# Kernel tuning notes

Hardware: AMD Instinct MI355X
Metric: run time of the kernel (lower is better)

The kernel has to match this reference:

```python
import jax, jax.numpy as jnp
import numpy as np

DIM = 1024
NUM_HEADS = 16


def setup_inputs() -> dict:
    key = jax.random.key(0)
    ks = jax.random.split(key, 8)
    B, N, C = 2, 2048, DIM
    x = jax.random.normal(ks[0], (B, N, C), dtype=jnp.float32)
    attn_mask = jnp.zeros((B, 1, N, N), dtype=jnp.float32)
    # learned parameters
    w_qkv = jax.random.normal(ks[1], (3 * C, C), dtype=jnp.float32) * (C ** -0.5)
    q_bias = jnp.zeros((C,), dtype=jnp.float32)
    k_bias = jnp.zeros((C,), dtype=jnp.float32)
    v_bias = jnp.zeros((C,), dtype=jnp.float32)
    w_proj = jax.random.normal(ks[2], (C, C), dtype=jnp.float32) * (C ** -0.5)
    b_proj = jnp.zeros((C,), dtype=jnp.float32)
    return {
        "x": x, "attn_mask": attn_mask,
        "w_qkv": w_qkv, "q_bias": q_bias, "k_bias": k_bias, "v_bias": v_bias,
        "w_proj": w_proj, "b_proj": b_proj,
        "num_heads": NUM_HEADS,
    }


def reference(x, attn_mask, w_qkv, q_bias, k_bias, v_bias, w_proj, b_proj, num_heads):
    B, N, C = x.shape
    H = num_heads
    hd = C // H
    scale = hd ** -0.5
    alpha = 32.0
    # fused qkv projection with concatenated biases
    qkv_bias = jnp.concatenate([q_bias, k_bias, v_bias])
    qkv = x @ w_qkv.T + qkv_bias                       # [B, N, 3C]
    qkv = qkv.reshape(B, N, 3, H, hd).transpose(2, 0, 3, 1, 4)  # [3, B, H, N, hd]
    q, k, v = qkv[0], qkv[1], qkv[2]
    # stabilization trick: scale q down by alpha, compute scores, re-scale after max-subtraction
    q = q * (scale / alpha)
    attn = jnp.einsum('bhld,bhmd->bhlm', q, k)         # [B, H, N, N]
    attn = (attn - jnp.max(attn, axis=-1, keepdims=True)) * alpha
    attn = attn + attn_mask                            # additive mask, broadcast over heads
    attn = jax.nn.softmax(attn, axis=-1)
    out = jnp.einsum('bhlm,bhmd->blhd', attn, v).reshape(B, N, C)
    out = out @ w_proj.T + b_proj
    return out
```

## Files before the change

kernel.cpp:

```cpp
#include <hip/hip_runtime.h>

typedef unsigned short u16;
typedef __bf16   bf16x8 __attribute__((ext_vector_type(8)));
typedef float    f32x4  __attribute__((ext_vector_type(4)));
typedef float    f32x16 __attribute__((ext_vector_type(16)));
typedef unsigned u32x4v __attribute__((ext_vector_type(4)));
typedef u16      u16x8  __attribute__((ext_vector_type(8)));

#define DEV __device__ __forceinline__

DEV u16 tobf(float f) {
  return __builtin_bit_cast(unsigned short, (__bf16)f);
}

DEV unsigned pack2(float a, float b) {
  return (unsigned)tobf(a) | ((unsigned)tobf(b) << 16);
}

DEV f32x4 fzero() { f32x4 z; z[0]=0.f; z[1]=0.f; z[2]=0.f; z[3]=0.f; return z; }

DEV void async_cp16(void* lds, const void* g) {
  __builtin_amdgcn_global_load_lds(
      (const __attribute__((address_space(1))) void*)g,
      (__attribute__((address_space(3))) void*)lds, 16, 0, 0);
}

DEV void cvt8(const float* __restrict__ in, u16* __restrict__ out, int i) {
  const float4* in4 = (const float4*)in;
  float4 a = in4[2*i], b = in4[2*i+1];
  u16x8 r;
  r[0]=tobf(a.x); r[1]=tobf(a.y); r[2]=tobf(a.z); r[3]=tobf(a.w);
  r[4]=tobf(b.x); r[5]=tobf(b.y); r[6]=tobf(b.z); r[7]=tobf(b.w);
  *(u16x8*)(out + 8*(size_t)i) = r;
}

__global__ __launch_bounds__(256)
void k_pre(const float* __restrict__ x, const float* __restrict__ wqkv,
           const float* __restrict__ wproj,
           u16* __restrict__ xb, u16* __restrict__ wqkvb, u16* __restrict__ wprojb,
           const u32x4v* __restrict__ mask, unsigned* __restrict__ flag)
{
  const int tid = blockIdx.x * blockDim.x + threadIdx.x;
  const int stride = gridDim.x * blockDim.x;
  for (int i = tid; i < 524288; i += stride) cvt8(x, xb, i);
  for (int i = tid; i < 393216; i += stride) cvt8(wqkv, wqkvb, i);
  for (int i = tid; i < 131072; i += stride) cvt8(wproj, wprojb, i);
  unsigned o = 0;
  for (int i = tid; i < 2097152; i += stride) {
    u32x4v v = mask[i];
    o |= v[0] | v[1] | v[2] | v[3];
  }
  if (o & 0x7fffffffu) atomicOr(flag, 1u);
}

template<int EPI>
__global__ __launch_bounds__(256)
void k_gemm_nt(const u16* __restrict__ A, const u16* __restrict__ B,
               int N, int K, int nbn,
               const float* __restrict__ bq, const float* __restrict__ bk,
               const float* __restrict__ bv,
               u16* __restrict__ qo, u16* __restrict__ ko, u16* __restrict__ vto,
               float* __restrict__ fo, const float* __restrict__ bp)
{
  __shared__ u16 sA[2][4096];
  __shared__ u16 sB[2][4096];

  const int tid  = threadIdx.x;
  const int lane = tid & 63;
  const int wave = tid >> 6;
  const int lr = lane & 15, lg = lane >> 4;
  const int wr = wave >> 1, wc = wave & 1;

  const int per = gridDim.x >> 3;
  const int bid = blockIdx.x;
  const int swz = (bid & 7) * per + (bid >> 3);
  const int bm0 = (swz / nbn) << 7;
  const int bn0 = (swz - (swz / nbn) * nbn) << 7;

  const size_t Kb = (size_t)K * 2;

  auto stage = [&](int buf, int kt) {
#pragma unroll
    for (int j = 0; j < 2; ++j) {
      int off = (tid + j * 256) << 4;
      int row = off >> 6;
      int ch  = (off & 63) >> 4;
      int gch = ch ^ (row & 3);
      async_cp16((char*)&sA[buf][0] + off,
                 (const char*)A + (size_t)(bm0 + row) * Kb + (size_t)kt * 64 + gch * 16);
      async_cp16((char*)&sB[buf][0] + off,
                 (const char*)B + (size_t)(bn0 + row) * Kb + (size_t)kt * 64 + gch * 16);
    }
  };

  f32x4 acc[4][4];
#pragma unroll
  for (int i = 0; i < 4; ++i)
#pragma unroll
    for (int j = 0; j < 4; ++j) acc[i][j] = fzero();

  const int nk = K >> 5;
  stage(0, 0);

  for (int kt = 0; kt < nk; ++kt) {
    const int cur = kt & 1;
    if (kt + 1 < nk) {
      stage(cur ^ 1, kt + 1);
      asm volatile("s_waitcnt vmcnt(4)" ::: "memory");
    } else {
      asm volatile("s_waitcnt vmcnt(0)" ::: "memory");
    }
    __builtin_amdgcn_s_barrier();
    __builtin_amdgcn_sched_barrier(0);

    bf16x8 af[4], bfr[4];
#pragma unroll
    for (int mi = 0; mi < 4; ++mi) {
      int row = (wr << 6) + (mi << 4) + lr;
      int addr = (row << 6) + ((lg ^ (row & 3)) << 4);
      af[mi] = *(const bf16x8*)((const char*)&sA[cur][0] + addr);
    }
#pragma unroll
    for (int ni = 0; ni < 4; ++ni) {
      int row = (wc << 6) + (ni << 4) + lr;
      int addr = (row << 6) + ((lg ^ (row & 3)) << 4);
      bfr[ni] = *(const bf16x8*)((const char*)&sB[cur][0] + addr);
    }
    __builtin_amdgcn_s_setprio(1);
#pragma unroll
    for (int mi = 0; mi < 4; ++mi)
#pragma unroll
      for (int ni = 0; ni < 4; ++ni)
        acc[mi][ni] = __builtin_amdgcn_mfma_f32_16x16x32_bf16(af[mi], bfr[ni], acc[mi][ni], 0, 0, 0);
    __builtin_amdgcn_s_setprio(0);

    __builtin_amdgcn_s_barrier();
  }

#pragma unroll
  for (int mi = 0; mi < 4; ++mi) {
#pragma unroll
    for (int ni = 0; ni < 4; ++ni) {
      int col = bn0 + (wc << 6) + (ni << 4) + lr;
      if (EPI == 0) {
        int s = col >> 10, hd = col & 1023;
        int h = hd >> 6, d = hd & 63;
        float bias = (s == 0 ? bq[hd] : (s == 1 ? bk[hd] : bv[hd]));
#pragma unroll
        for (int r = 0; r < 4; ++r) {
          int m = bm0 + (wr << 6) + (mi << 4) + (lg << 2) + r;
          int b = m >> 11, n = m & 2047;
          float v = acc[mi][ni][r] + bias;
          if (s == 0) v *= 0.125f;
          u16 val = tobf(v);
          size_t bh = (size_t)(b * 16 + h);
          if (s == 0)      qo[(bh * 2048 + n) * 64 + d] = val;
          else if (s == 1) ko[(bh * 2048 + n) * 64 + d] = val;
          else             vto[(bh * 64 + d) * 2048 + n] = val;
        }
      } else {
        float bias = bp[col];
#pragma unroll
        for (int r = 0; r < 4; ++r) {
          int m = bm0 + (wr << 6) + (mi << 4) + (lg << 2) + r;
          fo[(size_t)m * N + col] = acc[mi][ni][r] + bias;
        }
      }
    }
  }
}

__global__ __launch_bounds__(256)
void k_attn(const u16* __restrict__ qb, const u16* __restrict__ kb,
            const u16* __restrict__ vtb, u16* __restrict__ ao,
            const float* __restrict__ mask, const unsigned* __restrict__ flag)
{
  constexpr int N = 2048;
  constexpr int NTT = N / 64;
  __shared__ u16 sK[4][4096];
  __shared__ u16 sV[4][4096];

  const int tid  = threadIdx.x;
  const int lane = tid & 63;
  const int wave = tid >> 6;
  const int l31  = lane & 31;
  const int hi   = lane >> 5;

  const int bid  = blockIdx.x;
  const int xcd  = bid & 7, slot = bid >> 3;
  const int bh   = xcd + 8 * (slot >> 4);
  const int qt   = slot & 15;
  const int b    = bh >> 4, h = bh & 15;

  const u16* Kbh = kb  + (size_t)bh * N * 64;
  const u16* Vbh = vtb + (size_t)bh * 64 * N;
  const int q_lo = qt * 128 + wave * 32;
  const int qg   = q_lo + l31;

  bf16x8 qf[4];
  {
    const u16* qrow = qb + ((size_t)bh * N + qg) * 64;
#pragma unroll
    for (int ks = 0; ks < 4; ++ks)
      qf[ks] = *(const bf16x8*)(qrow + ks * 16 + hi * 8);
  }

  const unsigned use_mask = *flag;
  const float* maskb = mask + (size_t)b * N * N;

  float m_run = -INFINITY, lsum = 0.f;
  f32x16 o0, o1;
#pragma unroll
  for (int r = 0; r < 16; ++r) { o0[r] = 0.f; o1[r] = 0.f; }

  auto stage = [&](int buf, int kt) {
#pragma unroll
    for (int j = 0; j < 2; ++j) {
      int off = (tid + j * 256) << 4;
      int row = off >> 7;
      int ch  = (off & 127) >> 4;
      int gch = ch ^ (row & 7);
      async_cp16((char*)&sK[buf][0] + off,
                 (const char*)Kbh + (size_t)(kt * 64 + row) * 128 + gch * 16);
      async_cp16((char*)&sV[buf][0] + off,
                 (const char*)Vbh + (size_t)row * (N * 2) + (size_t)kt * 128 + gch * 16);
    }
  };

  stage(0, 0);
  stage(1, 1);

  const float L2E = 1.44269504088896340736f;

  for (int kt = 0; kt < NTT; ++kt) {
    const int cur = kt & 3;
    if (kt + 2 < NTT) stage((kt + 2) & 3, kt + 2);
    if (kt + 2 < NTT)      asm volatile("s_waitcnt vmcnt(8)" ::: "memory");
    else if (kt + 1 < NTT) asm volatile("s_waitcnt vmcnt(4)" ::: "memory");
    else                   asm volatile("s_waitcnt vmcnt(0)" ::: "memory");
    __builtin_amdgcn_s_barrier();
    __builtin_amdgcn_sched_barrier(0);

    const char* kbase = (const char*)&sK[cur][0];
    const char* vbase = (const char*)&sV[cur][0];

    f32x16 sc0, sc1;
#pragma unroll
    for (int r = 0; r < 16; ++r) { sc0[r] = 0.f; sc1[r] = 0.f; }

    __builtin_amdgcn_s_setprio(1);
#pragma unroll
    for (int ks = 0; ks < 4; ++ks) {
      int row0 = l31;
      int a0 = (row0 << 7) + ((((ks << 1) + hi) ^ (row0 & 7)) << 4);
      bf16x8 kf0 = *(const bf16x8*)(kbase + a0);
      sc0 = __builtin_amdgcn_mfma_f32_32x32x16_bf16(kf0, qf[ks], sc0, 0, 0, 0);
      int row1 = 32 + l31;
      int a1 = (row1 << 7) + ((((ks << 1) + hi) ^ (row1 & 7)) << 4);
      bf16x8 kf1 = *(const bf16x8*)(kbase + a1);
      sc1 = __builtin_amdgcn_mfma_f32_32x32x16_bf16(kf1, qf[ks], sc1, 0, 0, 0);
    }
    __builtin_amdgcn_s_setprio(0);

    if (use_mask) {
#pragma unroll
      for (int r = 0; r < 16; ++r) {
        int krow = (r & 3) + 8 * (r >> 2) + 4 * hi;
        sc0[r] += maskb[(size_t)qg * N + kt * 64 + krow];
        sc1[r] += maskb[(size_t)qg * N + kt * 64 + 32 + krow];
      }
    }

    float tmx[8];
#pragma unroll
    for (int r = 0; r < 8; ++r)
      tmx[r] = fmaxf(fmaxf(sc0[r], sc0[r + 8]), fmaxf(sc1[r], sc1[r + 8]));
#pragma unroll
    for (int r = 0; r < 4; ++r) tmx[r] = fmaxf(tmx[r], tmx[r + 4]);
    float pm = fmaxf(fmaxf(tmx[0], tmx[1]), fmaxf(tmx[2], tmx[3]));
    pm = fmaxf(pm, __shfl_xor(pm, 32, 64));

    if (__any(pm > m_run + 8.f)) {
      const float m_new = fmaxf(m_run, pm);
      const float f = __builtin_amdgcn_exp2f((m_run - m_new) * L2E);
      m_run = m_new;
#pragma unroll
      for (int r = 0; r < 16; ++r) {
        float fr = __shfl(f, (r & 3) + 8 * (r >> 2) + 4 * hi, 64);
        o0[r] *= fr; o1[r] *= fr;
      }
      lsum *= f;
    }

    const float mL2 = m_run * L2E;
    float rs0 = 0.f, rs1 = 0.f, rs2 = 0.f, rs3 = 0.f;
#pragma unroll
    for (int r = 0; r < 16; r += 4) {
      sc0[r]   = __builtin_amdgcn_exp2f(__builtin_fmaf(sc0[r],   L2E, -mL2));
      sc0[r+1] = __builtin_amdgcn_exp2f(__builtin_fmaf(sc0[r+1], L2E, -mL2));
      sc0[r+2] = __builtin_amdgcn_exp2f(__builtin_fmaf(sc0[r+2], L2E, -mL2));
      sc0[r+3] = __builtin_amdgcn_exp2f(__builtin_fmaf(sc0[r+3], L2E, -mL2));
      sc1[r]   = __builtin_amdgcn_exp2f(__builtin_fmaf(sc1[r],   L2E, -mL2));
      sc1[r+1] = __builtin_amdgcn_exp2f(__builtin_fmaf(sc1[r+1], L2E, -mL2));
      sc1[r+2] = __builtin_amdgcn_exp2f(__builtin_fmaf(sc1[r+2], L2E, -mL2));
      sc1[r+3] = __builtin_amdgcn_exp2f(__builtin_fmaf(sc1[r+3], L2E, -mL2));
      rs0 += sc0[r]   + sc1[r];
      rs1 += sc0[r+1] + sc1[r+1];
      rs2 += sc0[r+2] + sc1[r+2];
      rs3 += sc0[r+3] + sc1[r+3];
    }
    float rs = (rs0 + rs1) + (rs2 + rs3);
    rs += __shfl_xor(rs, 32, 64);
    lsum += rs;

    unsigned P32_0[8], P32_1[8];
#pragma unroll
    for (int tt = 0; tt < 8; ++tt) {
      P32_0[tt] = pack2(sc0[2 * tt], sc0[2 * tt + 1]);
      P32_1[tt] = pack2(sc1[2 * tt], sc1[2 * tt + 1]);
    }

    bf16x8 pa[4];
#pragma unroll
    for (int ks16 = 0; ks16 < 4; ++ks16) {
      const int b4 = (ks16 & 1) << 2;
      unsigned c0, c1, c2, c3;
      if (ks16 < 2) { c0 = P32_0[b4]; c2 = P32_0[b4+2]; c1 = P32_0[b4+1]; c3 = P32_0[b4+3]; }
      else          { c0 = P32_1[b4]; c2 = P32_1[b4+2]; c1 = P32_1[b4+1]; c3 = P32_1[b4+3]; }
      asm volatile("v_permlane32_swap_b32 %0, %1" : "+v"(c0), "+v"(c2));
      asm volatile("v_permlane32_swap_b32 %0, %1" : "+v"(c1), "+v"(c3));
      u32x4v w; w[0] = c0; w[1] = c1; w[2] = c2; w[3] = c3;
      pa[ks16] = __builtin_bit_cast(bf16x8, w);
    }

    __builtin_amdgcn_s_setprio(1);
#pragma unroll
    for (int ks16 = 0; ks16 < 4; ++ks16) {
      int row0 = l31;
      int a0 = (row0 << 7) + ((((ks16 << 1) + hi) ^ (row0 & 7)) << 4);
      bf16x8 vf0 = *(const bf16x8*)(vbase + a0);
      o0 = __builtin_amdgcn_mfma_f32_32x32x16_bf16(pa[ks16], vf0, o0, 0, 0, 0);
      int row1 = 32 + l31;
      int a1 = (row1 << 7) + ((((ks16 << 1) + hi) ^ (row1 & 7)) << 4);
      bf16x8 vf1 = *(const bf16x8*)(vbase + a1);
      o1 = __builtin_amdgcn_mfma_f32_32x32x16_bf16(pa[ks16], vf1, o1, 0, 0, 0);
    }
    __builtin_amdgcn_s_setprio(0);
  }

  const float inv = 1.0f / lsum;
#pragma unroll
  for (int r = 0; r < 16; ++r) {
    int idx = (r & 3) + 8 * (r >> 2) + 4 * hi;
    float ivr = __shfl(inv, idx, 64);
    int qrow = q_lo + idx;
    size_t base = ((size_t)(b * N + qrow)) * 1024 + h * 64;
    ao[base + l31]      = tobf(o0[r] * ivr);
    ao[base + 32 + l31] = tobf(o1[r] * ivr);
  }
}

extern "C" void kernel_launch(void* const* d_in, const int* in_sizes, int n_in,
                              void* d_out, int out_size, void* d_ws, size_t ws_size,
                              hipStream_t stream) {
  const float* x      = (const float*)d_in[0];
  const float* mask   = (const float*)d_in[1];
  const float* w_qkv  = (const float*)d_in[2];
  const float* q_bias = (const float*)d_in[3];
  const float* k_bias = (const float*)d_in[4];
  const float* v_bias = (const float*)d_in[5];
  const float* w_proj = (const float*)d_in[6];
  const float* b_proj = (const float*)d_in[7];
  float* out = (float*)d_out;

  const int B = 2, N = 2048, C = 1024;
  const int M = B * N;

  u16* ws     = (u16*)d_ws;
  u16* xb     = ws;
  u16* wqkvb  = ws + 4194304;
  u16* wprojb = ws + 7340032;
  u16* qbuf   = ws + 8388608;
  u16* kbuf   = ws + 12582912;
  u16* vtbuf  = ws + 16777216;
  unsigned* flag = (unsigned*)(ws + 20971520);
  u16* aob    = xb;

  hipMemsetAsync(flag, 0, 4, stream);
  k_pre<<<2048, 256, 0, stream>>>(x, w_qkv, w_proj, xb, wqkvb, wprojb,
                                  (const u32x4v*)mask, flag);

  k_gemm_nt<0><<<(M / 128) * (3 * C / 128), 256, 0, stream>>>(
      xb, wqkvb, 3 * C, C, 3 * C / 128,
      q_bias, k_bias, v_bias, qbuf, kbuf, vtbuf, nullptr, nullptr);

  k_attn<<<B * 16 * (N / 128), 256, 0, stream>>>(qbuf, kbuf, vtbuf, aob, mask, flag);

  k_gemm_nt<1><<<(M / 128) * (C / 128), 256, 0, stream>>>(
      aob, wprojb, C, C, C / 128,
      nullptr, nullptr, nullptr, nullptr, nullptr, nullptr, out, b_proj);
}
```

Before: 144.0 us.

## Software-pipeline attention loop: compute next tile's QK^T during current softmax/PV

Restructures the flash-attention inner loop so the QK^T MFMAs for tile t+1 are issued before the softmax and PV work for tile t, with score accumulators ping-ponged between two register sets. Wait counts are tightened so tile t+1 is resident in LDS before its scores are computed. The aim is to overlap matrix-core work with the exp/max/pack VALU work. It costs extra accumulator registers, which may reduce occupancy or cause spills.

```diff
diff --git a/kernel.cpp b/kernel.cpp
--- a/kernel.cpp
+++ b/kernel.cpp
@@ -227,41 +227,28 @@
     }
   };
 
-  stage(0, 0);
-  stage(1, 1);
-
-  const float L2E = 1.44269504088896340736f;
-
-  for (int kt = 0; kt < NTT; ++kt) {
-    const int cur = kt & 3;
-    if (kt + 2 < NTT) stage((kt + 2) & 3, kt + 2);
-    if (kt + 2 < NTT)      asm volatile("s_waitcnt vmcnt(8)" ::: "memory");
-    else if (kt + 1 < NTT) asm volatile("s_waitcnt vmcnt(4)" ::: "memory");
-    else                   asm volatile("s_waitcnt vmcnt(0)" ::: "memory");
-    __builtin_amdgcn_s_barrier();
-    __builtin_amdgcn_sched_barrier(0);
-
-    const char* kbase = (const char*)&sK[cur][0];
-    const char* vbase = (const char*)&sV[cur][0];
-
-    f32x16 sc0, sc1;
-#pragma unroll
-    for (int r = 0; r < 16; ++r) { sc0[r] = 0.f; sc1[r] = 0.f; }
-
+  auto qk = [&](int kt, f32x16& d0, f32x16& d1) {
+    const char* kbase = (const char*)&sK[kt & 3][0];
+#pragma unroll
+    for (int r = 0; r < 16; ++r) { d0[r] = 0.f; d1[r] = 0.f; }
     __builtin_amdgcn_s_setprio(1);
 #pragma unroll
     for (int ks = 0; ks < 4; ++ks) {
       int row0 = l31;
       int a0 = (row0 << 7) + ((((ks << 1) + hi) ^ (row0 & 7)) << 4);
       bf16x8 kf0 = *(const bf16x8*)(kbase + a0);
-      sc0 = __builtin_amdgcn_mfma_f32_32x32x16_bf16(kf0, qf[ks], sc0, 0, 0, 0);
+      d0 = __builtin_amdgcn_mfma_f32_32x32x16_bf16(kf0, qf[ks], d0, 0, 0, 0);
       int row1 = 32 + l31;
       int a1 = (row1 << 7) + ((((ks << 1) + hi) ^ (row1 & 7)) << 4);
       bf16x8 kf1 = *(const bf16x8*)(kbase + a1);
-      sc1 = __builtin_amdgcn_mfma_f32_32x32x16_bf16(kf1, qf[ks], sc1, 0, 0, 0);
+      d1 = __builtin_amdgcn_mfma_f32_32x32x16_bf16(kf1, qf[ks], d1, 0, 0, 0);
     }
     __builtin_amdgcn_s_setprio(0);
-
+  };
+
+  const float L2E = 1.44269504088896340736f;
+
+  auto smpv = [&](int kt, f32x16& sc0, f32x16& sc1) {
     if (use_mask) {
 #pragma unroll
       for (int r = 0; r < 16; ++r) {
@@ -333,6 +320,7 @@
       pa[ks16] = __builtin_bit_cast(bf16x8, w);
     }
 
+    const char* vbase = (const char*)&sV[kt & 3][0];
     __builtin_amdgcn_s_setprio(1);
 #pragma unroll
     for (int ks16 = 0; ks16 < 4; ++ks16) {
@@ -346,6 +334,31 @@
       o1 = __builtin_amdgcn_mfma_f32_32x32x16_bf16(pa[ks16], vf1, o1, 0, 0, 0);
     }
     __builtin_amdgcn_s_setprio(0);
+  };
+
+  stage(0, 0);
+  stage(1, 1);
+  asm volatile("s_waitcnt vmcnt(4)" ::: "memory");
+  __builtin_amdgcn_s_barrier();
+  __builtin_amdgcn_sched_barrier(0);
+
+  f32x16 scA0, scA1, scB0, scB1;
+  qk(0, scA0, scA1);
+
+#pragma unroll 2
+  for (int t = 0; t < NTT; ++t) {
+    if (t + 2 < NTT) stage((t + 2) & 3, t + 2);
+    if (t + 2 < NTT)      asm volatile("s_waitcnt vmcnt(4)" ::: "memory");
+    else                  asm volatile("s_waitcnt vmcnt(0)" ::: "memory");
+    __builtin_amdgcn_s_barrier();
+    __builtin_amdgcn_sched_barrier(0);
+
+    if (t + 1 < NTT) qk(t + 1, scB0, scB1);
+    smpv(t, scA0, scA1);
+
+    f32x16 u0 = scA0, u1 = scA1;
+    scA0 = scB0; scA1 = scB1;
+    scB0 = u0;  scB1 = u1;
   }
 
   const float inv = 1.0f / lsum;
```

Measured after the change: 145.2 us. No clear change (+0.9%).

## Split attention KV range across two blocks and merge partials in a new kernel

Applied to the files above, without the earlier changes.

Splits each query tile's key range into two halves handled by separate blocks, doubling the grid from 512 to 1024 blocks so more CUs are occupied. Each block writes an unnormalized-then-normalized partial output plus its row max and sum, and a new merge kernel combines the two halves with softmax rescaling. The K/V pipeline is reduced from a 4-buffer depth-2 prefetch with fine-grained waitcnt to double buffering with __syncthreads, and launch bounds request higher occupancy. This adds an extra kernel launch, extra global traffic for the partials, and bf16 rounding of intermediate partials.

```diff
diff --git a/kernel.cpp b/kernel.cpp
--- a/kernel.cpp
+++ b/kernel.cpp
@@ -11,6 +11,10 @@
 
 DEV u16 tobf(float f) {
   return __builtin_bit_cast(unsigned short, (__bf16)f);
+}
+
+DEV float frombf(u16 u) {
+  return (float)__builtin_bit_cast(__bf16, u);
 }
 
 DEV unsigned pack2(float a, float b) {
@@ -170,15 +174,15 @@
   }
 }
 
-__global__ __launch_bounds__(256)
+__global__ __launch_bounds__(256, 4)
 void k_attn(const u16* __restrict__ qb, const u16* __restrict__ kb,
-            const u16* __restrict__ vtb, u16* __restrict__ ao,
+            const u16* __restrict__ vtb, u16* __restrict__ pa,
+            float2* __restrict__ stats,
             const float* __restrict__ mask, const unsigned* __restrict__ flag)
 {
   constexpr int N = 2048;
-  constexpr int NTT = N / 64;
-  __shared__ u16 sK[4][4096];
-  __shared__ u16 sV[4][4096];
+  __shared__ u16 sK[2][4096];
+  __shared__ u16 sV[2][4096];
 
   const int tid  = threadIdx.x;
   const int lane = tid & 63;
@@ -188,9 +192,12 @@
 
   const int bid  = blockIdx.x;
   const int xcd  = bid & 7, slot = bid >> 3;
-  const int bh   = xcd + 8 * (slot >> 4);
-  const int qt   = slot & 15;
-  const int b    = bh >> 4, h = bh & 15;
+  const int g    = slot & 1;
+  const int s2   = slot >> 1;
+  const int bh   = xcd + 8 * (s2 >> 4);
+  const int qt   = s2 & 15;
+  const int b    = bh >> 4;
+  const int kt0  = g << 4;
 
   const u16* Kbh = kb  + (size_t)bh * N * 64;
   const u16* Vbh = vtb + (size_t)bh * 64 * N;
@@ -227,19 +234,15 @@
     }
   };
 
-  stage(0, 0);
-  stage(1, 1);
+  stage(0, kt0);
+  __syncthreads();
 
   const float L2E = 1.44269504088896340736f;
 
-  for (int kt = 0; kt < NTT; ++kt) {
-    const int cur = kt & 3;
-    if (kt + 2 < NTT) stage((kt + 2) & 3, kt + 2);
-    if (kt + 2 < NTT)      asm volatile("s_waitcnt vmcnt(8)" ::: "memory");
-    else if (kt + 1 < NTT) asm volatile("s_waitcnt vmcnt(4)" ::: "memory");
-    else                   asm volatile("s_waitcnt vmcnt(0)" ::: "memory");
-    __builtin_amdgcn_s_barrier();
-    __builtin_amdgcn_sched_barrier(0);
+  for (int tt = 0; tt < 16; ++tt) {
+    const int kt  = kt0 + tt;
+    const int cur = tt & 1;
+    if (tt + 1 < 16) stage(cur ^ 1, kt + 1);
 
     const char* kbase = (const char*)&sK[cur][0];
     const char* vbase = (const char*)&sV[cur][0];
@@ -315,12 +318,12 @@
 
     unsigned P32_0[8], P32_1[8];
 #pragma unroll
-    for (int tt = 0; tt < 8; ++tt) {
-      P32_0[tt] = pack2(sc0[2 * tt], sc0[2 * tt + 1]);
-      P32_1[tt] = pack2(sc1[2 * tt], sc1[2 * tt + 1]);
-    }
-
-    bf16x8 pa[4];
+    for (int pt = 0; pt < 8; ++pt) {
+      P32_0[pt] = pack2(sc0[2 * pt], sc0[2 * pt + 1]);
+      P32_1[pt] = pack2(sc1[2 * pt], sc1[2 * pt + 1]);
+    }
+
+    bf16x8 paf[4];
 #pragma unroll
     for (int ks16 = 0; ks16 < 4; ++ks16) {
       const int b4 = (ks16 & 1) << 2;
@@ -330,7 +333,7 @@
       asm volatile("v_permlane32_swap_b32 %0, %1" : "+v"(c0), "+v"(c2));
       asm volatile("v_permlane32_swap_b32 %0, %1" : "+v"(c1), "+v"(c3));
       u32x4v w; w[0] = c0; w[1] = c1; w[2] = c2; w[3] = c3;
-      pa[ks16] = __builtin_bit_cast(bf16x8, w);
+      paf[ks16] = __builtin_bit_cast(bf16x8, w);
     }
 
     __builtin_amdgcn_s_setprio(1);
@@ -339,25 +342,58 @@
       int row0 = l31;
       int a0 = (row0 << 7) + ((((ks16 << 1) + hi) ^ (row0 & 7)) << 4);
       bf16x8 vf0 = *(const bf16x8*)(vbase + a0);
-      o0 = __builtin_amdgcn_mfma_f32_32x32x16_bf16(pa[ks16], vf0, o0, 0, 0, 0);
+      o0 = __builtin_amdgcn_mfma_f32_32x32x16_bf16(paf[ks16], vf0, o0, 0, 0, 0);
       int row1 = 32 + l31;
       int a1 = (row1 << 7) + ((((ks16 << 1) + hi) ^ (row1 & 7)) << 4);
       bf16x8 vf1 = *(const bf16x8*)(vbase + a1);
-      o1 = __builtin_amdgcn_mfma_f32_32x32x16_bf16(pa[ks16], vf1, o1, 0, 0, 0);
+      o1 = __builtin_amdgcn_mfma_f32_32x32x16_bf16(paf[ks16], vf1, o1, 0, 0, 0);
     }
     __builtin_amdgcn_s_setprio(0);
+
+    __syncthreads();
   }
 
   const float inv = 1.0f / lsum;
+  u16* pab = pa + (size_t)g * 4194304;
 #pragma unroll
   for (int r = 0; r < 16; ++r) {
     int idx = (r & 3) + 8 * (r >> 2) + 4 * hi;
     float ivr = __shfl(inv, idx, 64);
     int qrow = q_lo + idx;
-    size_t base = ((size_t)(b * N + qrow)) * 1024 + h * 64;
-    ao[base + l31]      = tobf(o0[r] * ivr);
-    ao[base + 32 + l31] = tobf(o1[r] * ivr);
-  }
+    size_t base = ((size_t)bh * 2048 + qrow) * 64;
+    pab[base + l31]      = tobf(o0[r] * ivr);
+    pab[base + 32 + l31] = tobf(o1[r] * ivr);
+  }
+  if (hi == 0)
+    stats[g * 65536 + bh * 2048 + qg] = make_float2(m_run, lsum);
+}
+
+__global__ __launch_bounds__(256)
+void k_merge(const u16* __restrict__ pa, const float2* __restrict__ stats,
+             u16* __restrict__ ao)
+{
+  const float L2E = 1.44269504088896340736f;
+  int t = blockIdx.x * 256 + threadIdx.x;
+  int row = t >> 3;
+  int d8  = (t & 7) << 3;
+  float2 s0 = stats[row];
+  float2 s1 = stats[65536 + row];
+  float m  = fmaxf(s0.x, s1.x);
+  float a  = __builtin_amdgcn_exp2f((s0.x - m) * L2E) * s0.y;
+  float bb = __builtin_amdgcn_exp2f((s1.x - m) * L2E) * s1.y;
+  float inv = 1.0f / (a + bb);
+  float w0 = a * inv, w1 = bb * inv;
+
+  bf16x8 v0 = *(const bf16x8*)(pa + (size_t)row * 64 + d8);
+  bf16x8 v1 = *(const bf16x8*)(pa + 4194304 + (size_t)row * 64 + d8);
+  u16x8 r;
+#pragma unroll
+  for (int j = 0; j < 8; ++j)
+    r[j] = tobf(w0 * (float)v0[j] + w1 * (float)v1[j]);
+
+  int bh = row >> 11, n = row & 2047;
+  int b = bh >> 4, h = bh & 15;
+  *(u16x8*)(ao + ((size_t)(b * 2048 + n)) * 1024 + h * 64 + d8) = r;
 }
 
 extern "C" void kernel_launch(void* const* d_in, const int* in_sizes, int n_in,
@@ -384,6 +420,8 @@
   u16* kbuf   = ws + 12582912;
   u16* vtbuf  = ws + 16777216;
   unsigned* flag = (unsigned*)(ws + 20971520);
+  u16* pabuf  = ws + 20972032;
+  float2* statsbuf = (float2*)(ws + 4194304);
   u16* aob    = xb;
 
   hipMemsetAsync(flag, 0, 4, stream);
@@ -394,7 +432,10 @@
       xb, wqkvb, 3 * C, C, 3 * C / 128,
       q_bias, k_bias, v_bias, qbuf, kbuf, vtbuf, nullptr, nullptr);
 
-  k_attn<<<B * 16 * (N / 128), 256, 0, stream>>>(qbuf, kbuf, vtbuf, aob, mask, flag);
+  k_attn<<<B * 16 * (N / 128) * 2, 256, 0, stream>>>(
+      qbuf, kbuf, vtbuf, pabuf, statsbuf, mask, flag);
+
+  k_merge<<<2048, 256, 0, stream>>>(pabuf, statsbuf, aob);
 
   k_gemm_nt<1><<<(M / 128) * (C / 128), 256, 0, stream>>>(
       aob, wprojb, C, C, C / 128,
```

Result: slower. 152.3 us (+5.8%).
